# Performance work log

Measured on AMD Instinct MI355X. Metric: run time of the kernel, lower is better.

Reference implementation:

```python
import jax, jax.numpy as jnp
import numpy as np

N_NODES = 100000


def _gcn_norm(edge_index, num_nodes):
    # Add self-loops, then symmetric normalization D^-1/2 A D^-1/2 (PyG gcn_norm).
    loops = jnp.arange(num_nodes, dtype=edge_index.dtype)
    src = jnp.concatenate([edge_index[0], loops])
    dst = jnp.concatenate([edge_index[1], loops])
    ew = jnp.ones(src.shape[0], dtype=jnp.float32)
    deg = jax.ops.segment_sum(ew, dst, num_segments=num_nodes)
    dinv = jnp.where(deg > 0, jax.lax.rsqrt(deg), 0.0)
    norm = dinv[src] * ew * dinv[dst]
    return src, dst, norm


def _prop_gcn_conv(x, W, b, src, dst, norm, num_nodes, prop_nums):
    # PropGCNConv: linear transform once, then prop_nums hops of normalized
    # sparse propagation (gather from src, scale, scatter-add to dst), + bias.
    x = x @ W
    for _ in range(prop_nums):
        msgs = x[src] * norm[:, None]              # [E, d]
        x = jax.ops.segment_sum(msgs, dst, num_segments=num_nodes)
    return x + b


def setup_inputs() -> dict:
    key = jax.random.key(0)
    k1, k2, k3, k4 = jax.random.split(key, 4)
    in_dim, hid_dim, num_classes = 128, 64, 40
    n_edges = 800000
    x = jax.random.normal(k1, (N_NODES, in_dim), dtype=jnp.float32)
    W0 = jax.random.normal(k2, (in_dim, hid_dim), dtype=jnp.float32) * (1.0 / np.sqrt(in_dim))
    b0 = jnp.zeros((hid_dim,), dtype=jnp.float32)
    Wc = jax.random.normal(k3, (hid_dim, num_classes), dtype=jnp.float32) * (1.0 / np.sqrt(hid_dim))
    bc = jnp.zeros((num_classes,), dtype=jnp.float32)
    edge_index = jax.random.randint(k4, (2, n_edges), 0, N_NODES, dtype=jnp.int64)
    return {"x": x, "W0": W0, "b0": b0, "Wc": Wc, "bc": bc,
            "edge_index": edge_index, "prop_nums": 30}


def reference(x, W0, b0, Wc, bc, edge_index, prop_nums):
    n = x.shape[0]
    src, dst, norm = _gcn_norm(edge_index, n)
    # feat_bottleneck: conv -> relu -> dropout (eval mode -> identity)
    h = _prop_gcn_conv(x, W0, b0, src, dst, norm, n, prop_nums)
    h = jax.nn.relu(h)
    # feat_classifier: single-hop PropGCNConv
    out = _prop_gcn_conv(h, Wc, bc, src, dst, norm, n, 1)
    return out
```

## Files before the change

kernel.cpp:

```cpp
#include <hip/hip_runtime.h>

#define NN  100000
#define NE  800000
#define NNZ 900000
#define IN_DIM 128
#define HID 64
#define NC  40
#define HOPS 30

typedef _Float16 half8 __attribute__((ext_vector_type(8)));


__global__ void count_edges_k(const int* __restrict__ dst, int* __restrict__ cnt) {
    int e = blockIdx.x * blockDim.x + threadIdx.x;
    if (e < NE) atomicAdd(&cnt[dst[e]], 1);
}

__global__ void dinv_k(const int* __restrict__ cnt, float* __restrict__ dinv) {
    int i = blockIdx.x * blockDim.x + threadIdx.x;
    if (i < NN) dinv[i] = rsqrtf((float)(cnt[i] + 1));
}

__global__ void scan_blocks_k(const int* __restrict__ cnt, int* __restrict__ rp,
                              int* __restrict__ partials) {
    __shared__ int s[256];
    int tid = threadIdx.x;
    int i = blockIdx.x * 256 + tid;
    int v = (i < NN) ? (cnt[i] + 1) : 0;
    s[tid] = v;
    __syncthreads();
    for (int off = 1; off < 256; off <<= 1) {
        int t = (tid >= off) ? s[tid - off] : 0;
        __syncthreads();
        s[tid] += t;
        __syncthreads();
    }
    if (i < NN) rp[i] = s[tid] - v;
    if (tid == 255) partials[blockIdx.x] = s[255];
}

__global__ void scan_partials_k(int* __restrict__ partials, int nblk) {
    __shared__ int s[512];
    int tid = threadIdx.x;
    int v = (tid < nblk) ? partials[tid] : 0;
    s[tid] = v;
    __syncthreads();
    for (int off = 1; off < 512; off <<= 1) {
        int t = (tid >= off) ? s[tid - off] : 0;
        __syncthreads();
        s[tid] += t;
        __syncthreads();
    }
    if (tid < nblk) partials[tid] = s[tid] - v;
}

__global__ void add_offsets_k(int* __restrict__ rp, const int* __restrict__ partials) {
    int i = blockIdx.x * 256 + threadIdx.x;
    if (i < NN) rp[i] += partials[blockIdx.x];
    if (i == 0) rp[NN] = NNZ;
}

__global__ void fill_csr_k(const int* __restrict__ src, const int* __restrict__ dst,
                           const float* __restrict__ dinv, const int* __restrict__ rp,
                           int* __restrict__ cnt, int2* __restrict__ cv) {
    int e = blockIdx.x * blockDim.x + threadIdx.x;
    if (e >= NNZ) return;
    int pos;
    int2 p;
    if (e < NE) {
        int s = src[e], d = dst[e];
        float nv = dinv[s] * dinv[d];
        int old = atomicAdd(&cnt[d], -1);
        pos = rp[d] + old - 1;
        p.x = s;
        p.y = __float_as_int(nv);
    } else {
        int i = e - NE;
        pos = rp[i + 1] - 1;
        p.x = i;
        p.y = __float_as_int(dinv[i] * dinv[i]);
    }
    cv[pos] = p;
}


__global__ void __launch_bounds__(256) gemm1_k(const float* __restrict__ x,
                                               const float* __restrict__ W,
                                               _Float16* __restrict__ out) {
    int t = threadIdx.x;
    int cq = __builtin_amdgcn_readfirstlane(t >> 6);
    int node = blockIdx.x * 64 + (t & 63);
    int nc = node < NN ? node : NN - 1;
    const float4* xr = (const float4*)(x + (size_t)nc * IN_DIM);
    const float* Wq = W + cq * 16;
    float acc[16];
#pragma unroll
    for (int c = 0; c < 16; ++c) acc[c] = 0.f;
#pragma unroll 4
    for (int k4 = 0; k4 < IN_DIM / 4; ++k4) {
        float4 xv = xr[k4];
#pragma unroll
        for (int kk = 0; kk < 4; ++kk) {
            float xs = (kk == 0) ? xv.x : (kk == 1) ? xv.y : (kk == 2) ? xv.z : xv.w;
            const float4* wr = (const float4*)(Wq + (k4 * 4 + kk) * HID);
#pragma unroll
            for (int c4 = 0; c4 < 4; ++c4) {
                float4 wv = wr[c4];
                acc[c4 * 4 + 0] = fmaf(xs, wv.x, acc[c4 * 4 + 0]);
                acc[c4 * 4 + 1] = fmaf(xs, wv.y, acc[c4 * 4 + 1]);
                acc[c4 * 4 + 2] = fmaf(xs, wv.z, acc[c4 * 4 + 2]);
                acc[c4 * 4 + 3] = fmaf(xs, wv.w, acc[c4 * 4 + 3]);
            }
        }
    }
    if (node < NN) {
        half8* o = (half8*)(out + (size_t)node * HID + cq * 16);
        half8 r0, r1;
#pragma unroll
        for (int j = 0; j < 8; ++j) {
            r0[j] = (_Float16)acc[j];
            r1[j] = (_Float16)acc[j + 8];
        }
        o[0] = r0;
        o[1] = r1;
    }
}

__global__ void prop64_k(const _Float16* __restrict__ xin, _Float16* __restrict__ xout,
                         const int* __restrict__ rp, const int2* __restrict__ cv) {
    int wid  = threadIdx.x >> 6;
    int lane = threadIdx.x & 63;
    int n    = lane >> 5;
    int s    = (lane >> 3) & 3;
    int f    = lane & 7;
    int node = blockIdx.x * 8 + wid * 2 + n;
    int beg = rp[node], end = rp[node + 1];
    const half8* x8 = (const half8*)xin;
    const long long* cvl = (const long long*)cv;
    float a0 = 0.f, a1 = 0.f, a2 = 0.f, a3 = 0.f, a4 = 0.f, a5 = 0.f, a6 = 0.f, a7 = 0.f;
    for (int e = beg + s; e < end; e += 16) {
        int  e1 = e + 4,  e2 = e + 8,  e3 = e + 12;
        bool p1 = e1 < end, p2 = e2 < end, p3 = e3 < end;
        long long l0 = __builtin_nontemporal_load(&cvl[e]);
        long long l1 = __builtin_nontemporal_load(&cvl[p1 ? e1 : beg]);
        long long l2 = __builtin_nontemporal_load(&cvl[p2 ? e2 : beg]);
        long long l3 = __builtin_nontemporal_load(&cvl[p3 ? e3 : beg]);
        int c0 = (int)l0, c1 = (int)l1, c2 = (int)l2, c3 = (int)l3;
        float v0 = __int_as_float((int)(l0 >> 32));
        float v1 = p1 ? __int_as_float((int)(l1 >> 32)) : 0.f;
        float v2 = p2 ? __int_as_float((int)(l2 >> 32)) : 0.f;
        float v3 = p3 ? __int_as_float((int)(l3 >> 32)) : 0.f;
        half8 x0 = x8[(size_t)c0 * 8 + f];
        half8 x1 = x8[(size_t)c1 * 8 + f];
        half8 x2 = x8[(size_t)c2 * 8 + f];
        half8 x3 = x8[(size_t)c3 * 8 + f];
        a0 += v0 * (float)x0[0] + v1 * (float)x1[0] + v2 * (float)x2[0] + v3 * (float)x3[0];
        a1 += v0 * (float)x0[1] + v1 * (float)x1[1] + v2 * (float)x2[1] + v3 * (float)x3[1];
        a2 += v0 * (float)x0[2] + v1 * (float)x1[2] + v2 * (float)x2[2] + v3 * (float)x3[2];
        a3 += v0 * (float)x0[3] + v1 * (float)x1[3] + v2 * (float)x2[3] + v3 * (float)x3[3];
        a4 += v0 * (float)x0[4] + v1 * (float)x1[4] + v2 * (float)x2[4] + v3 * (float)x3[4];
        a5 += v0 * (float)x0[5] + v1 * (float)x1[5] + v2 * (float)x2[5] + v3 * (float)x3[5];
        a6 += v0 * (float)x0[6] + v1 * (float)x1[6] + v2 * (float)x2[6] + v3 * (float)x3[6];
        a7 += v0 * (float)x0[7] + v1 * (float)x1[7] + v2 * (float)x2[7] + v3 * (float)x3[7];
    }
#pragma unroll
    for (int m = 8; m <= 16; m <<= 1) {
        a0 += __shfl_xor(a0, m); a1 += __shfl_xor(a1, m);
        a2 += __shfl_xor(a2, m); a3 += __shfl_xor(a3, m);
        a4 += __shfl_xor(a4, m); a5 += __shfl_xor(a5, m);
        a6 += __shfl_xor(a6, m); a7 += __shfl_xor(a7, m);
    }
    if (s == 0) {
        half8 r;
        r[0] = (_Float16)a0; r[1] = (_Float16)a1; r[2] = (_Float16)a2; r[3] = (_Float16)a3;
        r[4] = (_Float16)a4; r[5] = (_Float16)a5; r[6] = (_Float16)a6; r[7] = (_Float16)a7;
        ((half8*)xout)[(size_t)node * 8 + f] = r;
    }
}

__global__ void __launch_bounds__(256, 4) gemm2_k(const _Float16* __restrict__ h,
                                                  const float* __restrict__ b0,
                                                  const float* __restrict__ Wc,
                                                  _Float16* __restrict__ g) {
    __shared__ float Wcs[HID * NC];
    __shared__ float b0s[HID];
    int t = threadIdx.x;
    for (int i = t; i < HID * NC / 4; i += 256)
        ((float4*)Wcs)[i] = ((const float4*)Wc)[i];
    if (t < HID) b0s[t] = b0[t];
    __syncthreads();
    int node = blockIdx.x * 256 + t;
    if (node >= NN) return;
    const half8* hr = (const half8*)(h + (size_t)node * HID);
    float acc[NC];
#pragma unroll
    for (int c = 0; c < NC; ++c) acc[c] = 0.f;
#pragma unroll
    for (int j = 0; j < 8; ++j) {
        half8 hv = hr[j];
#pragma unroll
        for (int m = 0; m < 8; ++m) {
            int k = j * 8 + m;
            float fv = fmaxf((float)hv[m] + b0s[k], 0.f);
            const float4* wr = (const float4*)(Wcs + k * NC);
#pragma unroll
            for (int c4 = 0; c4 < NC / 4; ++c4) {
                float4 wv = wr[c4];
                acc[c4 * 4 + 0] = fmaf(fv, wv.x, acc[c4 * 4 + 0]);
                acc[c4 * 4 + 1] = fmaf(fv, wv.y, acc[c4 * 4 + 1]);
                acc[c4 * 4 + 2] = fmaf(fv, wv.z, acc[c4 * 4 + 2]);
                acc[c4 * 4 + 3] = fmaf(fv, wv.w, acc[c4 * 4 + 3]);
            }
        }
    }
    half8* go = (half8*)(g + (size_t)node * 64);
#pragma unroll
    for (int j = 0; j < 5; ++j) {
        half8 r;
#pragma unroll
        for (int m = 0; m < 8; ++m) r[m] = (_Float16)acc[j * 8 + m];
        go[j] = r;
    }
}

__global__ void prop40_k(const _Float16* __restrict__ g, float* __restrict__ out,
                         const int* __restrict__ rp, const int2* __restrict__ cv,
                         const float* __restrict__ bc) {
    int t = blockIdx.x * 256 + threadIdx.x;
    int node = t >> 6;
    int lane = threadIdx.x & 63;
    int s = lane >> 3;
    int f = lane & 7;
    int beg = rp[node], end = rp[node + 1];
    const half8* g8 = (const half8*)g;
    const long long* cvl = (const long long*)cv;
    bool act = f < 5;
    float a0 = 0.f, a1 = 0.f, a2 = 0.f, a3 = 0.f, a4 = 0.f, a5 = 0.f, a6 = 0.f, a7 = 0.f;
    for (int e = beg + s; e < end; e += 16) {
        int  e1 = e + 8;
        bool p1 = e1 < end;
        long long l0 = __builtin_nontemporal_load(&cvl[e]);
        long long l1 = __builtin_nontemporal_load(&cvl[p1 ? e1 : beg]);
        int c0 = (int)l0, c1 = (int)l1;
        float v0 = __int_as_float((int)(l0 >> 32));
        float v1 = p1 ? __int_as_float((int)(l1 >> 32)) : 0.f;
        if (act) {
            half8 x0 = g8[(size_t)c0 * 8 + f];
            half8 x1 = g8[(size_t)c1 * 8 + f];
            a0 += v0 * (float)x0[0] + v1 * (float)x1[0];
            a1 += v0 * (float)x0[1] + v1 * (float)x1[1];
            a2 += v0 * (float)x0[2] + v1 * (float)x1[2];
            a3 += v0 * (float)x0[3] + v1 * (float)x1[3];
            a4 += v0 * (float)x0[4] + v1 * (float)x1[4];
            a5 += v0 * (float)x0[5] + v1 * (float)x1[5];
            a6 += v0 * (float)x0[6] + v1 * (float)x1[6];
            a7 += v0 * (float)x0[7] + v1 * (float)x1[7];
        }
    }
#pragma unroll
    for (int m = 8; m <= 32; m <<= 1) {
        a0 += __shfl_xor(a0, m); a1 += __shfl_xor(a1, m);
        a2 += __shfl_xor(a2, m); a3 += __shfl_xor(a3, m);
        a4 += __shfl_xor(a4, m); a5 += __shfl_xor(a5, m);
        a6 += __shfl_xor(a6, m); a7 += __shfl_xor(a7, m);
    }
    if (s == 0 && act) {
        float* o = out + (size_t)node * NC + f * 8;
        o[0] = a0 + bc[f * 8 + 0];
        o[1] = a1 + bc[f * 8 + 1];
        o[2] = a2 + bc[f * 8 + 2];
        o[3] = a3 + bc[f * 8 + 3];
        o[4] = a4 + bc[f * 8 + 4];
        o[5] = a5 + bc[f * 8 + 5];
        o[6] = a6 + bc[f * 8 + 6];
        o[7] = a7 + bc[f * 8 + 7];
    }
}


extern "C" void kernel_launch(void* const* d_in, const int* in_sizes, int n_in,
                              void* d_out, int out_size, void* d_ws, size_t ws_size,
                              hipStream_t stream) {
    const float* x  = (const float*)d_in[0];
    const float* W0 = (const float*)d_in[1];
    const float* b0 = (const float*)d_in[2];
    const float* Wc = (const float*)d_in[3];
    const float* bc = (const float*)d_in[4];
    const int*   ei = (const int*)d_in[5];
    const int* src = ei;
    const int* dst = ei + NE;

    char* ws = (char*)d_ws;
    size_t off = 0;
    auto alloc = [&](size_t bytes) -> void* {
        void* p = ws + off;
        off = (off + bytes + 255) & ~(size_t)255;
        return p;
    };
    float* dinv     = (float*)alloc((size_t)NN * 4);
    int*   rp       = (int*)  alloc((size_t)(NN + 1) * 4);
    int*   cnt      = (int*)  alloc((size_t)NN * 4);
    int*   partials = (int*)  alloc(512 * 4);
    int2*  cvp      = (int2*) alloc((size_t)NNZ * 8);
    _Float16* XA    = (_Float16*)alloc((size_t)NN * HID * 2);
    _Float16* XB    = (_Float16*)alloc((size_t)NN * HID * 2);
    _Float16* G     = (_Float16*)alloc((size_t)NN * 64 * 2);

    const int nblk_n = (NN + 255) / 256;
    const int nblk_z = (NNZ + 255) / 256;

    hipMemsetAsync(cnt, 0, (size_t)NN * 4, stream);
    count_edges_k<<<(NE + 255) / 256, 256, 0, stream>>>(dst, cnt);
    dinv_k       <<<nblk_n, 256, 0, stream>>>(cnt, dinv);
    scan_blocks_k<<<nblk_n, 256, 0, stream>>>(cnt, rp, partials);
    scan_partials_k<<<1, 512, 0, stream>>>(partials, nblk_n);
    add_offsets_k<<<nblk_n, 256, 0, stream>>>(rp, partials);
    fill_csr_k   <<<nblk_z, 256, 0, stream>>>(src, dst, dinv, rp, cnt, cvp);

    gemm1_k<<<(NN + 63) / 64, 256, 0, stream>>>(x, W0, XA);

    _Float16* a = XA;
    _Float16* b = XB;
    for (int hop = 0; hop < HOPS; ++hop) {
        prop64_k<<<NN / 8, 256, 0, stream>>>(a, b, rp, cvp);
        _Float16* tmp2 = a; a = b; b = tmp2;
    }

    gemm2_k<<<nblk_n, 256, 0, stream>>>(a, b0, Wc, G);
    prop40_k<<<NN * HID / 256, 256, 0, stream>>>(G, (float*)d_out, rp, cvp, bc);
}
```

Baseline: 925.0 us.

## Factor symmetric normalization into node scaling, store column-only CSR

Rewrites D^-1/2 A D^-1/2 propagation so edges carry no weights. The features are pre-scaled by dinv and each hop's output is scaled by dinv^2, so the CSR stores only 4-byte column indices instead of 8-byte (col, weight) pairs. Padded edges point to a zeroed dummy row instead of using zero weights. G is also packed to 40 columns, which cuts gather bandwidth in the final hop. The change halves edge-array traffic per hop and removes the per-edge multiplies. It adds fp16 range and precision risk because the scaled intermediates are stored and then rescaled by 1/dinv in gemm2.

```diff
diff --git a/kernel.cpp b/kernel.cpp
--- a/kernel.cpp
+++ b/kernel.cpp
@@ -61,31 +61,28 @@
 }
 
 __global__ void fill_csr_k(const int* __restrict__ src, const int* __restrict__ dst,
-                           const float* __restrict__ dinv, const int* __restrict__ rp,
-                           int* __restrict__ cnt, int2* __restrict__ cv) {
+                           const int* __restrict__ rp, int* __restrict__ cnt,
+                           int* __restrict__ col) {
     int e = blockIdx.x * blockDim.x + threadIdx.x;
     if (e >= NNZ) return;
-    int pos;
-    int2 p;
+    int pos, c;
     if (e < NE) {
         int s = src[e], d = dst[e];
-        float nv = dinv[s] * dinv[d];
         int old = atomicAdd(&cnt[d], -1);
         pos = rp[d] + old - 1;
-        p.x = s;
-        p.y = __float_as_int(nv);
+        c = s;
     } else {
         int i = e - NE;
         pos = rp[i + 1] - 1;
-        p.x = i;
-        p.y = __float_as_int(dinv[i] * dinv[i]);
-    }
-    cv[pos] = p;
+        c = i;
+    }
+    col[pos] = c;
 }
 
 
 __global__ void __launch_bounds__(256) gemm1_k(const float* __restrict__ x,
                                                const float* __restrict__ W,
+                                               const float* __restrict__ dinv,
                                                _Float16* __restrict__ out) {
     int t = threadIdx.x;
     int cq = __builtin_amdgcn_readfirstlane(t >> 6);
@@ -114,12 +111,13 @@
         }
     }
     if (node < NN) {
+        float dv = dinv[node];
         half8* o = (half8*)(out + (size_t)node * HID + cq * 16);
         half8 r0, r1;
 #pragma unroll
         for (int j = 0; j < 8; ++j) {
-            r0[j] = (_Float16)acc[j];
-            r1[j] = (_Float16)acc[j + 8];
+            r0[j] = (_Float16)(acc[j] * dv);
+            r1[j] = (_Float16)(acc[j + 8] * dv);
         }
         o[0] = r0;
         o[1] = r1;
@@ -127,7 +125,8 @@
 }
 
 __global__ void prop64_k(const _Float16* __restrict__ xin, _Float16* __restrict__ xout,
-                         const int* __restrict__ rp, const int2* __restrict__ cv) {
+                         const int* __restrict__ rp, const int* __restrict__ col,
+                         const float* __restrict__ dinv) {
     int wid  = threadIdx.x >> 6;
     int lane = threadIdx.x & 63;
     int n    = lane >> 5;
@@ -136,32 +135,29 @@
     int node = blockIdx.x * 8 + wid * 2 + n;
     int beg = rp[node], end = rp[node + 1];
     const half8* x8 = (const half8*)xin;
-    const long long* cvl = (const long long*)cv;
     float a0 = 0.f, a1 = 0.f, a2 = 0.f, a3 = 0.f, a4 = 0.f, a5 = 0.f, a6 = 0.f, a7 = 0.f;
     for (int e = beg + s; e < end; e += 16) {
         int  e1 = e + 4,  e2 = e + 8,  e3 = e + 12;
         bool p1 = e1 < end, p2 = e2 < end, p3 = e3 < end;
-        long long l0 = __builtin_nontemporal_load(&cvl[e]);
-        long long l1 = __builtin_nontemporal_load(&cvl[p1 ? e1 : beg]);
-        long long l2 = __builtin_nontemporal_load(&cvl[p2 ? e2 : beg]);
-        long long l3 = __builtin_nontemporal_load(&cvl[p3 ? e3 : beg]);
-        int c0 = (int)l0, c1 = (int)l1, c2 = (int)l2, c3 = (int)l3;
-        float v0 = __int_as_float((int)(l0 >> 32));
-        float v1 = p1 ? __int_as_float((int)(l1 >> 32)) : 0.f;
-        float v2 = p2 ? __int_as_float((int)(l2 >> 32)) : 0.f;
-        float v3 = p3 ? __int_as_float((int)(l3 >> 32)) : 0.f;
+        int c0 = col[e];
+        int c1 = col[p1 ? e1 : e];
+        int c2 = col[p2 ? e2 : e];
+        int c3 = col[p3 ? e3 : e];
+        c1 = p1 ? c1 : NN;
+        c2 = p2 ? c2 : NN;
+        c3 = p3 ? c3 : NN;
         half8 x0 = x8[(size_t)c0 * 8 + f];
         half8 x1 = x8[(size_t)c1 * 8 + f];
         half8 x2 = x8[(size_t)c2 * 8 + f];
         half8 x3 = x8[(size_t)c3 * 8 + f];
-        a0 += v0 * (float)x0[0] + v1 * (float)x1[0] + v2 * (float)x2[0] + v3 * (float)x3[0];
-        a1 += v0 * (float)x0[1] + v1 * (float)x1[1] + v2 * (float)x2[1] + v3 * (float)x3[1];
-        a2 += v0 * (float)x0[2] + v1 * (float)x1[2] + v2 * (float)x2[2] + v3 * (float)x3[2];
-        a3 += v0 * (float)x0[3] + v1 * (float)x1[3] + v2 * (float)x2[3] + v3 * (float)x3[3];
-        a4 += v0 * (float)x0[4] + v1 * (float)x1[4] + v2 * (float)x2[4] + v3 * (float)x3[4];
-        a5 += v0 * (float)x0[5] + v1 * (float)x1[5] + v2 * (float)x2[5] + v3 * (float)x3[5];
-        a6 += v0 * (float)x0[6] + v1 * (float)x1[6] + v2 * (float)x2[6] + v3 * (float)x3[6];
-        a7 += v0 * (float)x0[7] + v1 * (float)x1[7] + v2 * (float)x2[7] + v3 * (float)x3[7];
+        a0 += (float)x0[0] + (float)x1[0] + (float)x2[0] + (float)x3[0];
+        a1 += (float)x0[1] + (float)x1[1] + (float)x2[1] + (float)x3[1];
+        a2 += (float)x0[2] + (float)x1[2] + (float)x2[2] + (float)x3[2];
+        a3 += (float)x0[3] + (float)x1[3] + (float)x2[3] + (float)x3[3];
+        a4 += (float)x0[4] + (float)x1[4] + (float)x2[4] + (float)x3[4];
+        a5 += (float)x0[5] + (float)x1[5] + (float)x2[5] + (float)x3[5];
+        a6 += (float)x0[6] + (float)x1[6] + (float)x2[6] + (float)x3[6];
+        a7 += (float)x0[7] + (float)x1[7] + (float)x2[7] + (float)x3[7];
     }
 #pragma unroll
     for (int m = 8; m <= 16; m <<= 1) {
@@ -171,9 +167,13 @@
         a6 += __shfl_xor(a6, m); a7 += __shfl_xor(a7, m);
     }
     if (s == 0) {
+        float dv = dinv[node];
+        float d2 = dv * dv;
         half8 r;
-        r[0] = (_Float16)a0; r[1] = (_Float16)a1; r[2] = (_Float16)a2; r[3] = (_Float16)a3;
-        r[4] = (_Float16)a4; r[5] = (_Float16)a5; r[6] = (_Float16)a6; r[7] = (_Float16)a7;
+        r[0] = (_Float16)(a0 * d2); r[1] = (_Float16)(a1 * d2);
+        r[2] = (_Float16)(a2 * d2); r[3] = (_Float16)(a3 * d2);
+        r[4] = (_Float16)(a4 * d2); r[5] = (_Float16)(a5 * d2);
+        r[6] = (_Float16)(a6 * d2); r[7] = (_Float16)(a7 * d2);
         ((half8*)xout)[(size_t)node * 8 + f] = r;
     }
 }
@@ -181,6 +181,7 @@
 __global__ void __launch_bounds__(256, 4) gemm2_k(const _Float16* __restrict__ h,
                                                   const float* __restrict__ b0,
                                                   const float* __restrict__ Wc,
+                                                  const float* __restrict__ dinv,
                                                   _Float16* __restrict__ g) {
     __shared__ float Wcs[HID * NC];
     __shared__ float b0s[HID];
@@ -191,6 +192,8 @@
     __syncthreads();
     int node = blockIdx.x * 256 + t;
     if (node >= NN) return;
+    float dv = dinv[node];
+    float sdeg = 1.0f / dv;
     const half8* hr = (const half8*)(h + (size_t)node * HID);
     float acc[NC];
 #pragma unroll
@@ -201,7 +204,7 @@
 #pragma unroll
         for (int m = 0; m < 8; ++m) {
             int k = j * 8 + m;
-            float fv = fmaxf((float)hv[m] + b0s[k], 0.f);
+            float fv = fmaxf(fmaf((float)hv[m], sdeg, b0s[k]), 0.f);
             const float4* wr = (const float4*)(Wcs + k * NC);
 #pragma unroll
             for (int c4 = 0; c4 < NC / 4; ++c4) {
@@ -213,19 +216,19 @@
             }
         }
     }
-    half8* go = (half8*)(g + (size_t)node * 64);
+    half8* go = (half8*)(g + (size_t)node * NC);
 #pragma unroll
     for (int j = 0; j < 5; ++j) {
         half8 r;
 #pragma unroll
-        for (int m = 0; m < 8; ++m) r[m] = (_Float16)acc[j * 8 + m];
+        for (int m = 0; m < 8; ++m) r[m] = (_Float16)(acc[j * 8 + m] * dv);
         go[j] = r;
     }
 }
 
 __global__ void prop40_k(const _Float16* __restrict__ g, float* __restrict__ out,
-                         const int* __restrict__ rp, const int2* __restrict__ cv,
-                         const float* __restrict__ bc) {
+                         const int* __restrict__ rp, const int* __restrict__ col,
+                         const float* __restrict__ dinv, const float* __restrict__ bc) {
     int t = blockIdx.x * 256 + threadIdx.x;
     int node = t >> 6;
     int lane = threadIdx.x & 63;
@@ -233,28 +236,25 @@
     int f = lane & 7;
     int beg = rp[node], end = rp[node + 1];
     const half8* g8 = (const half8*)g;
-    const long long* cvl = (const long long*)cv;
     bool act = f < 5;
     float a0 = 0.f, a1 = 0.f, a2 = 0.f, a3 = 0.f, a4 = 0.f, a5 = 0.f, a6 = 0.f, a7 = 0.f;
     for (int e = beg + s; e < end; e += 16) {
         int  e1 = e + 8;
         bool p1 = e1 < end;
-        long long l0 = __builtin_nontemporal_load(&cvl[e]);
-        long long l1 = __builtin_nontemporal_load(&cvl[p1 ? e1 : beg]);
-        int c0 = (int)l0, c1 = (int)l1;
-        float v0 = __int_as_float((int)(l0 >> 32));
-        float v1 = p1 ? __int_as_float((int)(l1 >> 32)) : 0.f;
+        int c0 = col[e];
+        int c1 = col[p1 ? e1 : e];
+        c1 = p1 ? c1 : NN;
         if (act) {
-            half8 x0 = g8[(size_t)c0 * 8 + f];
-            half8 x1 = g8[(size_t)c1 * 8 + f];
-            a0 += v0 * (float)x0[0] + v1 * (float)x1[0];
-            a1 += v0 * (float)x0[1] + v1 * (float)x1[1];
-            a2 += v0 * (float)x0[2] + v1 * (float)x1[2];
-            a3 += v0 * (float)x0[3] + v1 * (float)x1[3];
-            a4 += v0 * (float)x0[4] + v1 * (float)x1[4];
-            a5 += v0 * (float)x0[5] + v1 * (float)x1[5];
-            a6 += v0 * (float)x0[6] + v1 * (float)x1[6];
-            a7 += v0 * (float)x0[7] + v1 * (float)x1[7];
+            half8 x0 = g8[(size_t)c0 * 5 + f];
+            half8 x1 = g8[(size_t)c1 * 5 + f];
+            a0 += (float)x0[0] + (float)x1[0];
+            a1 += (float)x0[1] + (float)x1[1];
+            a2 += (float)x0[2] + (float)x1[2];
+            a3 += (float)x0[3] + (float)x1[3];
+            a4 += (float)x0[4] + (float)x1[4];
+            a5 += (float)x0[5] + (float)x1[5];
+            a6 += (float)x0[6] + (float)x1[6];
+            a7 += (float)x0[7] + (float)x1[7];
         }
     }
 #pragma unroll
@@ -265,15 +265,16 @@
         a6 += __shfl_xor(a6, m); a7 += __shfl_xor(a7, m);
     }
     if (s == 0 && act) {
+        float dv = dinv[node];
         float* o = out + (size_t)node * NC + f * 8;
-        o[0] = a0 + bc[f * 8 + 0];
-        o[1] = a1 + bc[f * 8 + 1];
-        o[2] = a2 + bc[f * 8 + 2];
-        o[3] = a3 + bc[f * 8 + 3];
-        o[4] = a4 + bc[f * 8 + 4];
-        o[5] = a5 + bc[f * 8 + 5];
-        o[6] = a6 + bc[f * 8 + 6];
-        o[7] = a7 + bc[f * 8 + 7];
+        o[0] = fmaf(a0, dv, bc[f * 8 + 0]);
+        o[1] = fmaf(a1, dv, bc[f * 8 + 1]);
+        o[2] = fmaf(a2, dv, bc[f * 8 + 2]);
+        o[3] = fmaf(a3, dv, bc[f * 8 + 3]);
+        o[4] = fmaf(a4, dv, bc[f * 8 + 4]);
+        o[5] = fmaf(a5, dv, bc[f * 8 + 5]);
+        o[6] = fmaf(a6, dv, bc[f * 8 + 6]);
+        o[7] = fmaf(a7, dv, bc[f * 8 + 7]);
     }
 }
 
@@ -301,31 +302,34 @@
     int*   rp       = (int*)  alloc((size_t)(NN + 1) * 4);
     int*   cnt      = (int*)  alloc((size_t)NN * 4);
     int*   partials = (int*)  alloc(512 * 4);
-    int2*  cvp      = (int2*) alloc((size_t)NNZ * 8);
-    _Float16* XA    = (_Float16*)alloc((size_t)NN * HID * 2);
-    _Float16* XB    = (_Float16*)alloc((size_t)NN * HID * 2);
-    _Float16* G     = (_Float16*)alloc((size_t)NN * 64 * 2);
+    int*   col      = (int*)  alloc((size_t)NNZ * 4);
+    _Float16* XA    = (_Float16*)alloc((size_t)(NN + 1) * HID * 2);
+    _Float16* XB    = (_Float16*)alloc((size_t)(NN + 1) * HID * 2);
+    _Float16* G     = (_Float16*)alloc((size_t)(NN + 1) * NC * 2);
 
     const int nblk_n = (NN + 255) / 256;
     const int nblk_z = (NNZ + 255) / 256;
 
     hipMemsetAsync(cnt, 0, (size_t)NN * 4, stream);
+    hipMemsetAsync(XA + (size_t)NN * HID, 0, HID * 2, stream);
+    hipMemsetAsync(XB + (size_t)NN * HID, 0, HID * 2, stream);
+    hipMemsetAsync(G  + (size_t)NN * NC,  0, NC * 2, stream);
     count_edges_k<<<(NE + 255) / 256, 256, 0, stream>>>(dst, cnt);
     dinv_k       <<<nblk_n, 256, 0, stream>>>(cnt, dinv);
     scan_blocks_k<<<nblk_n, 256, 0, stream>>>(cnt, rp, partials);
     scan_partials_k<<<1, 512, 0, stream>>>(partials, nblk_n);
     add_offsets_k<<<nblk_n, 256, 0, stream>>>(rp, partials);
-    fill_csr_k   <<<nblk_z, 256, 0, stream>>>(src, dst, dinv, rp, cnt, cvp);
-
-    gemm1_k<<<(NN + 63) / 64, 256, 0, stream>>>(x, W0, XA);
+    fill_csr_k   <<<nblk_z, 256, 0, stream>>>(src, dst, rp, cnt, col);
+
+    gemm1_k<<<(NN + 63) / 64, 256, 0, stream>>>(x, W0, dinv, XA);
 
     _Float16* a = XA;
     _Float16* b = XB;
     for (int hop = 0; hop < HOPS; ++hop) {
-        prop64_k<<<NN / 8, 256, 0, stream>>>(a, b, rp, cvp);
+        prop64_k<<<NN / 8, 256, 0, stream>>>(a, b, rp, col, dinv);
         _Float16* tmp2 = a; a = b; b = tmp2;
     }
 
-    gemm2_k<<<nblk_n, 256, 0, stream>>>(a, b0, Wc, G);
-    prop40_k<<<NN * HID / 256, 256, 0, stream>>>(G, (float*)d_out, rp, cvp, bc);
-}
+    gemm2_k<<<nblk_n, 256, 0, stream>>>(a, b0, Wc, dinv, G);
+    prop40_k<<<NN * HID / 256, 256, 0, stream>>>(G, (float*)d_out, rp, col, dinv, bc);
+}
```

After: 868.7 us. 6.1% less time.
